# Kernel tuning notes

Measured on AMD Instinct MI355X. Metric: run time of the kernel, lower is better.

Reference implementation:

```python
import jax, jax.numpy as jnp
import numpy as np

DIM = 1024
NUM_HEADS = 16
HEAD_DIM = DIM // NUM_HEADS
SCALE = 1.0 / float(np.sqrt(HEAD_DIM))


def setup_inputs() -> dict:
    key = jax.random.key(0)
    ks = jax.random.split(key, 5)
    B, S = 2, 2048
    x = jax.random.normal(ks[0], (B, S, DIM), dtype=jnp.float32)
    qkv_w = jax.random.normal(ks[1], (3 * DIM, DIM), dtype=jnp.float32) * (1.0 / np.sqrt(DIM))
    qkv_b = jax.random.normal(ks[2], (3 * DIM,), dtype=jnp.float32) * 0.02
    proj_w = jax.random.normal(ks[3], (DIM, DIM), dtype=jnp.float32) * (1.0 / np.sqrt(DIM))
    proj_b = jax.random.normal(ks[4], (DIM,), dtype=jnp.float32) * 0.02
    return {"x": x, "qkv_w": qkv_w, "qkv_b": qkv_b, "proj_w": proj_w, "proj_b": proj_b}


def reference(x, qkv_w, qkv_b, proj_w, proj_b):
    B, S, _ = x.shape
    # qkv projection: (B,S,3*DIM) -> (3, B, H, S, Dh)
    qkv = x @ qkv_w.T + qkv_b
    qkv = qkv.reshape(B, S, 3, NUM_HEADS, HEAD_DIM).transpose(2, 0, 3, 1, 4)
    q, k, v = qkv[0], qkv[1], qkv[2]
    # scaled dot-product attention (full score matrix, as in the original)
    scores = jnp.einsum('bhqd,bhkd->bhqk', q, k) * SCALE
    attn = jax.nn.softmax(scores, axis=-1)
    out = jnp.einsum('bhqk,bhkd->bhqd', attn, v)  # (B,H,S,Dh)
    out = out.transpose(0, 2, 1, 3).reshape(B, S, DIM)
    return out @ proj_w.T + proj_b
```

## Files before the change

### kernel.cpp

```cpp
#include <hip/hip_runtime.h>

#define DIM_ 1024
#define NH_ 16
#define HD_ 64
#define B_ 2
#define S_ 2048
#define M_ (B_ * S_)
#define NQKV_ (3 * DIM_)

typedef __attribute__((ext_vector_type(8))) __bf16 bf16x8;
typedef __attribute__((ext_vector_type(4))) __bf16 bf16x4;
typedef __attribute__((ext_vector_type(4))) float f32x4;

__device__ __forceinline__ void gl_lds16(const void* g, void* l) {
  __builtin_amdgcn_global_load_lds(
      (__attribute__((address_space(1))) void*)const_cast<void*>(g),
      (__attribute__((address_space(3))) void*)l, 16, 0, 0);
}

#define N4_X 1048576
#define N4_W1 786432
#define N4_W2 262144
__global__ __launch_bounds__(256) void cast_all(const float* __restrict__ x,
                                                const float* __restrict__ w1,
                                                const float* __restrict__ w2,
                                                __bf16* __restrict__ xb,
                                                __bf16* __restrict__ w1b,
                                                __bf16* __restrict__ w2b) {
  int i = blockIdx.x * 256 + threadIdx.x;
  const int stride = gridDim.x * 256;
  for (; i < N4_X + N4_W1 + N4_W2; i += stride) {
    const float4* src;
    bf16x4* dst;
    int j;
    if (i < N4_X) { src = (const float4*)x; dst = (bf16x4*)xb; j = i; }
    else if (i < N4_X + N4_W1) { src = (const float4*)w1; dst = (bf16x4*)w1b; j = i - N4_X; }
    else { src = (const float4*)w2; dst = (bf16x4*)w2b; j = i - (N4_X + N4_W1); }
    float4 v = src[j];
    bf16x4 o;
    o[0] = (__bf16)v.x; o[1] = (__bf16)v.y; o[2] = (__bf16)v.z; o[3] = (__bf16)v.w;
    dst[j] = o;
  }
}

template <int MODE>
__global__ __launch_bounds__(256) void gemm_bt(const __bf16* __restrict__ A,
                                               const __bf16* __restrict__ Bw,
                                               const float* __restrict__ bias,
                                               __bf16* __restrict__ Qp, __bf16* __restrict__ Kp,
                                               __bf16* __restrict__ Vt, float* __restrict__ Cout) {
  constexpr int KD = 1024;
  __shared__ __bf16 As[128 * 64];
  __shared__ __bf16 Bs[128 * 64];
  const int tid = threadIdx.x;
  const int lane = tid & 63;
  const int wave = tid >> 6;
  const int quad = lane >> 4;
  const int r16 = lane & 15;
  const int wm = wave >> 1;
  const int wn = wave & 1;
  const int m0 = blockIdx.y * 128;
  const int n0 = blockIdx.x * 128;

  const f32x4 fz = {0.f, 0.f, 0.f, 0.f};
  f32x4 acc[4][4];
#pragma unroll
  for (int i = 0; i < 4; ++i)
#pragma unroll
    for (int j = 0; j < 4; ++j) acc[i][j] = fz;

  const __bf16* ga[4];
  const __bf16* gb[4];
  __bf16 *la[4], *lb[4];
#pragma unroll
  for (int i = 0; i < 4; ++i) {
    const int c = tid + i * 256;
    const int r = c >> 3, cc = c & 7;
    const int col = ((cc ^ (r & 7)) * 8);
    ga[i] = A + (size_t)(m0 + r) * KD + col;
    gb[i] = Bw + (size_t)(n0 + r) * KD + col;
    la[i] = &As[c * 8];
    lb[i] = &Bs[c * 8];
  }

  for (int kt = 0; kt < KD / 64; ++kt) {
    __syncthreads();
#pragma unroll
    for (int i = 0; i < 4; ++i) {
      gl_lds16(ga[i], la[i]); ga[i] += 64;
      gl_lds16(gb[i], lb[i]); gb[i] += 64;
    }
    __syncthreads();

    bf16x8 af[2][4], bfr[2][4];
#pragma unroll
    for (int sub = 0; sub < 2; ++sub) {
      const int ch = ((sub * 4 + quad) ^ (r16 & 7)) * 8;
#pragma unroll
      for (int mt = 0; mt < 4; ++mt)
        af[sub][mt] = *(const bf16x8*)&As[(wm * 64 + mt * 16 + r16) * 64 + ch];
#pragma unroll
      for (int nt = 0; nt < 4; ++nt)
        bfr[sub][nt] = *(const bf16x8*)&Bs[(wn * 64 + nt * 16 + r16) * 64 + ch];
    }
#pragma unroll
    for (int sub = 0; sub < 2; ++sub)
#pragma unroll
      for (int mt = 0; mt < 4; ++mt)
#pragma unroll
        for (int nt = 0; nt < 4; ++nt)
          acc[mt][nt] =
              __builtin_amdgcn_mfma_f32_16x16x32_bf16(af[sub][mt], bfr[sub][nt], acc[mt][nt], 0, 0, 0);
  }

  if (MODE == 0) {
#pragma unroll
    for (int nt = 0; nt < 4; ++nt) {
      const int n = n0 + wn * 64 + nt * 16 + r16;
      const int sel = n >> 10;
      const int h = (n >> 6) & 15;
      const int dh = n & 63;
      const float bs = bias[n];
      if (sel == 2) {
#pragma unroll
        for (int mt = 0; mt < 4; ++mt) {
          const int m = m0 + wm * 64 + mt * 16 + quad * 4;
          const int b = m >> 11;
          const int s = m & 2047;
          const int slot = (s & ~31) | (((s >> 2) & 3) << 3) | (((s >> 4) & 1) << 2);
          bf16x4 ov;
#pragma unroll
          for (int r = 0; r < 4; ++r) ov[r] = (__bf16)(acc[mt][nt][r] + bs);
          *(bf16x4*)&Vt[((size_t)((b * NH_ + h) * HD_ + dh)) * S_ + slot] = ov;
        }
      } else {
        __bf16* dst = (sel == 0) ? Qp : Kp;
        const float mul = (sel == 0) ? 0.18033688011112042f : 1.0f;
#pragma unroll
        for (int mt = 0; mt < 4; ++mt) {
#pragma unroll
          for (int r = 0; r < 4; ++r) {
            const int m = m0 + wm * 64 + mt * 16 + quad * 4 + r;
            const int b = m >> 11;
            const int s = m & 2047;
            dst[((size_t)((b * NH_ + h) * S_ + s)) * HD_ + dh] =
                (__bf16)((acc[mt][nt][r] + bs) * mul);
          }
        }
      }
    }
  } else {
#pragma unroll
    for (int nt = 0; nt < 4; ++nt) {
      const int n = n0 + wn * 64 + nt * 16 + r16;
      const float bs = bias[n];
#pragma unroll
      for (int mt = 0; mt < 4; ++mt) {
#pragma unroll
        for (int r = 0; r < 4; ++r) {
          const int m = m0 + wm * 64 + mt * 16 + quad * 4 + r;
          Cout[(size_t)m * DIM_ + n] = acc[mt][nt][r] + bs;
        }
      }
    }
  }
}

__global__ __launch_bounds__(512) void attn(const __bf16* __restrict__ Qp,
                                            const __bf16* __restrict__ Kp,
                                            const __bf16* __restrict__ Vtp,
                                            __bf16* __restrict__ ctx) {
  __shared__ __bf16 Ks[2][128 * 64];
  __shared__ __bf16 Vs[2][64 * 128];
  const int tid = threadIdx.x;
  const int lane = tid & 63;
  const int wave = tid >> 6;
  const int quad = lane >> 4;
  const int r16 = lane & 15;
  const int bh = blockIdx.y;
  const int q0 = blockIdx.x * 128;
  const int qrow = q0 + wave * 16 + r16;

  const __bf16* qb = Qp + ((size_t)bh * S_ + qrow) * HD_;
  const bf16x8 qf0 = *(const bf16x8*)(qb + quad * 8);
  const bf16x8 qf1 = *(const bf16x8*)(qb + 32 + quad * 8);

  const f32x4 fz = {0.f, 0.f, 0.f, 0.f};
  f32x4 o[4];
#pragma unroll
  for (int d = 0; d < 4; ++d) o[d] = fz;
  float lsum = 0.f;

  const __bf16* gk[2];
  const __bf16* gv[2];
  int lofs[2];
#pragma unroll
  for (int i = 0; i < 2; ++i) {
    const int c = tid + i * 512;
    const int kr = c >> 3, kc = c & 7;
    gk[i] = Kp + ((size_t)bh * S_ + kr) * HD_ + ((kc ^ (kr & 7)) * 8);
    const int vr = c >> 4, vc = c & 15;
    gv[i] = Vtp + ((size_t)bh * HD_ + vr) * S_ + ((vc ^ (vr & 15)) * 8);
    lofs[i] = c * 8;
  }

#pragma unroll
  for (int i = 0; i < 2; ++i) {
    gl_lds16(gk[i], &Ks[0][lofs[i]]); gk[i] += 128 * HD_;
    gl_lds16(gv[i], &Vs[0][lofs[i]]); gv[i] += 128;
  }

  for (int kt = 0; kt < S_ / 128; ++kt) {
    const int cb = kt & 1;
    __syncthreads();
    if (kt + 1 < S_ / 128) {
#pragma unroll
      for (int i = 0; i < 2; ++i) {
        gl_lds16(gk[i], &Ks[cb ^ 1][lofs[i]]); gk[i] += 128 * HD_;
        gl_lds16(gv[i], &Vs[cb ^ 1][lofs[i]]); gv[i] += 128;
      }
    }

    f32x4 sa[8];
#pragma unroll
    for (int mt = 0; mt < 8; ++mt) {
      const int row = mt * 16 + r16;
      bf16x8 k0 = *(const bf16x8*)&Ks[cb][row * 64 + ((quad ^ (row & 7)) * 8)];
      bf16x8 k1 = *(const bf16x8*)&Ks[cb][row * 64 + (((4 + quad) ^ (row & 7)) * 8)];
      f32x4 t = fz;
      t = __builtin_amdgcn_mfma_f32_16x16x32_bf16(k0, qf0, t, 0, 0, 0);
      t = __builtin_amdgcn_mfma_f32_16x16x32_bf16(k1, qf1, t, 0, 0, 0);
      sa[mt] = t;
    }

    bf16x8 pf[4];
#pragma unroll
    for (int ks = 0; ks < 4; ++ks)
#pragma unroll
      for (int r = 0; r < 4; ++r) {
        float p0 = __builtin_amdgcn_exp2f(sa[2 * ks][r]);
        float p1 = __builtin_amdgcn_exp2f(sa[2 * ks + 1][r]);
        lsum += p0 + p1;
        pf[ks][r] = (__bf16)p0;
        pf[ks][4 + r] = (__bf16)p1;
      }

#pragma unroll
    for (int ks = 0; ks < 4; ++ks)
#pragma unroll
      for (int dt = 0; dt < 4; ++dt) {
        const int row = dt * 16 + r16;
        bf16x8 va = *(const bf16x8*)&Vs[cb][row * 128 + (((4 * ks + quad) ^ (row & 15)) * 8)];
        o[dt] = __builtin_amdgcn_mfma_f32_16x16x32_bf16(va, pf[ks], o[dt], 0, 0, 0);
      }
  }

  lsum += __shfl_xor(lsum, 16);
  lsum += __shfl_xor(lsum, 32);
  const float inv = 1.0f / lsum;
  const int b = bh >> 4, h = bh & 15;
  const int s = q0 + wave * 16 + r16;
#pragma unroll
  for (int dt = 0; dt < 4; ++dt) {
    bf16x4 ov;
#pragma unroll
    for (int r = 0; r < 4; ++r) ov[r] = (__bf16)(o[dt][r] * inv);
    *(bf16x4*)&ctx[((size_t)(b * S_ + s)) * DIM_ + h * 64 + dt * 16 + quad * 4] = ov;
  }
}

extern "C" void kernel_launch(void* const* d_in, const int* in_sizes, int n_in, void* d_out,
                              int out_size, void* d_ws, size_t ws_size, hipStream_t stream) {
  const float* x = (const float*)d_in[0];
  const float* qkv_w = (const float*)d_in[1];
  const float* qkv_b = (const float*)d_in[2];
  const float* proj_w = (const float*)d_in[3];
  const float* proj_b = (const float*)d_in[4];
  float* out = (float*)d_out;

  char* ws = (char*)d_ws;
  __bf16* Xb = (__bf16*)(ws);
  __bf16* Wb = (__bf16*)(ws + 8388608);
  __bf16* Pb = (__bf16*)(ws + 14680064);
  __bf16* Qp = (__bf16*)(ws + 16777216);
  __bf16* Kp = (__bf16*)(ws + 25165824);
  __bf16* Vt = (__bf16*)(ws + 33554432);
  __bf16* Cx = (__bf16*)(ws + 41943040);

  cast_all<<<2048, 256, 0, stream>>>(x, qkv_w, proj_w, Xb, Wb, Pb);
  gemm_bt<0><<<dim3(NQKV_ / 128, M_ / 128), 256, 0, stream>>>(Xb, Wb, qkv_b, Qp, Kp, Vt, nullptr);
  attn<<<dim3(S_ / 128, 32), 512, 0, stream>>>(Qp, Kp, Vt, Cx);
  gemm_bt<1><<<dim3(DIM_ / 128, M_ / 128), 256, 0, stream>>>(Cx, Pb, proj_b, nullptr, nullptr,
                                                             nullptr, out);
}
```

Baseline: 186.0 us.

## Use 8-wave GEMM blocks and smaller M tiles for output projection

The bf16 GEMM kernel now runs 512 threads (8 waves) per block instead of 256, so each wave owns a smaller slice of M (MT 16-row tiles). The M tile size becomes a template parameter, and the output projection uses BM=64 to double its grid. Global-to-LDS loads are merged into one loop shared by A and B, and fragment loads are interleaved per k-substep to cut register pressure. The aim is more waves and blocks in flight to hide latency, at the cost of less register-level reuse per wave and more B-tile reloads for the smaller projection tiles.

```diff
diff --git a/kernel.cpp b/kernel.cpp
--- a/kernel.cpp
+++ b/kernel.cpp
@@ -43,15 +43,19 @@
   }
 }
 
-template <int MODE>
-__global__ __launch_bounds__(256) void gemm_bt(const __bf16* __restrict__ A,
-                                               const __bf16* __restrict__ Bw,
-                                               const float* __restrict__ bias,
-                                               __bf16* __restrict__ Qp, __bf16* __restrict__ Kp,
-                                               __bf16* __restrict__ Vt, float* __restrict__ Cout) {
+template <int MODE, int BM>
+__global__ __launch_bounds__(512, 4) void gemm_bt(const __bf16* __restrict__ A,
+                                                  const __bf16* __restrict__ Bw,
+                                                  const float* __restrict__ bias,
+                                                  __bf16* __restrict__ Qp, __bf16* __restrict__ Kp,
+                                                  __bf16* __restrict__ Vt,
+                                                  float* __restrict__ Cout) {
   constexpr int KD = 1024;
-  __shared__ __bf16 As[128 * 64];
-  __shared__ __bf16 Bs[128 * 64];
+  constexpr int BN = 128;
+  constexpr int MT = BM / 64;
+  constexpr int NC = (BM + BN) / 64;
+  __shared__ __bf16 As[BM * 64];
+  __shared__ __bf16 Bs[BN * 64];
   const int tid = threadIdx.x;
   const int lane = tid & 63;
   const int wave = tid >> 6;
@@ -59,58 +63,56 @@
   const int r16 = lane & 15;
   const int wm = wave >> 1;
   const int wn = wave & 1;
-  const int m0 = blockIdx.y * 128;
-  const int n0 = blockIdx.x * 128;
+  const int m0 = blockIdx.y * BM;
+  const int n0 = blockIdx.x * BN;
 
   const f32x4 fz = {0.f, 0.f, 0.f, 0.f};
-  f32x4 acc[4][4];
-#pragma unroll
-  for (int i = 0; i < 4; ++i)
+  f32x4 acc[MT][4];
+#pragma unroll
+  for (int i = 0; i < MT; ++i)
 #pragma unroll
     for (int j = 0; j < 4; ++j) acc[i][j] = fz;
 
-  const __bf16* ga[4];
-  const __bf16* gb[4];
-  __bf16 *la[4], *lb[4];
-#pragma unroll
-  for (int i = 0; i < 4; ++i) {
-    const int c = tid + i * 256;
-    const int r = c >> 3, cc = c & 7;
-    const int col = ((cc ^ (r & 7)) * 8);
-    ga[i] = A + (size_t)(m0 + r) * KD + col;
-    gb[i] = Bw + (size_t)(n0 + r) * KD + col;
-    la[i] = &As[c * 8];
-    lb[i] = &Bs[c * 8];
+  const __bf16* gp[NC];
+  __bf16* lp[NC];
+#pragma unroll
+  for (int i = 0; i < NC; ++i) {
+    const int c = tid + i * 512;
+    if (c < BM * 8) {
+      const int r = c >> 3, cc = c & 7;
+      gp[i] = A + (size_t)(m0 + r) * KD + ((cc ^ (r & 7)) * 8);
+      lp[i] = &As[c * 8];
+    } else {
+      const int c2 = c - BM * 8;
+      const int r = c2 >> 3, cc = c2 & 7;
+      gp[i] = Bw + (size_t)(n0 + r) * KD + ((cc ^ (r & 7)) * 8);
+      lp[i] = &Bs[c2 * 8];
+    }
   }
 
   for (int kt = 0; kt < KD / 64; ++kt) {
     __syncthreads();
 #pragma unroll
-    for (int i = 0; i < 4; ++i) {
-      gl_lds16(ga[i], la[i]); ga[i] += 64;
-      gl_lds16(gb[i], lb[i]); gb[i] += 64;
-    }
+    for (int i = 0; i < NC; ++i) { gl_lds16(gp[i], lp[i]); gp[i] += 64; }
     __syncthreads();
 
-    bf16x8 af[2][4], bfr[2][4];
 #pragma unroll
     for (int sub = 0; sub < 2; ++sub) {
       const int ch = ((sub * 4 + quad) ^ (r16 & 7)) * 8;
-#pragma unroll
-      for (int mt = 0; mt < 4; ++mt)
-        af[sub][mt] = *(const bf16x8*)&As[(wm * 64 + mt * 16 + r16) * 64 + ch];
+      bf16x8 af[MT], bfr[4];
+#pragma unroll
+      for (int mt = 0; mt < MT; ++mt)
+        af[mt] = *(const bf16x8*)&As[(wm * MT * 16 + mt * 16 + r16) * 64 + ch];
 #pragma unroll
       for (int nt = 0; nt < 4; ++nt)
-        bfr[sub][nt] = *(const bf16x8*)&Bs[(wn * 64 + nt * 16 + r16) * 64 + ch];
-    }
-#pragma unroll
-    for (int sub = 0; sub < 2; ++sub)
-#pragma unroll
-      for (int mt = 0; mt < 4; ++mt)
+        bfr[nt] = *(const bf16x8*)&Bs[(wn * 64 + nt * 16 + r16) * 64 + ch];
+#pragma unroll
+      for (int mt = 0; mt < MT; ++mt)
 #pragma unroll
         for (int nt = 0; nt < 4; ++nt)
           acc[mt][nt] =
-              __builtin_amdgcn_mfma_f32_16x16x32_bf16(af[sub][mt], bfr[sub][nt], acc[mt][nt], 0, 0, 0);
+              __builtin_amdgcn_mfma_f32_16x16x32_bf16(af[mt], bfr[nt], acc[mt][nt], 0, 0, 0);
+    }
   }
 
   if (MODE == 0) {
@@ -123,8 +125,8 @@
       const float bs = bias[n];
       if (sel == 2) {
 #pragma unroll
-        for (int mt = 0; mt < 4; ++mt) {
-          const int m = m0 + wm * 64 + mt * 16 + quad * 4;
+        for (int mt = 0; mt < MT; ++mt) {
+          const int m = m0 + wm * MT * 16 + mt * 16 + quad * 4;
           const int b = m >> 11;
           const int s = m & 2047;
           const int slot = (s & ~31) | (((s >> 2) & 3) << 3) | (((s >> 4) & 1) << 2);
@@ -137,10 +139,10 @@
         __bf16* dst = (sel == 0) ? Qp : Kp;
         const float mul = (sel == 0) ? 0.18033688011112042f : 1.0f;
 #pragma unroll
-        for (int mt = 0; mt < 4; ++mt) {
+        for (int mt = 0; mt < MT; ++mt) {
 #pragma unroll
           for (int r = 0; r < 4; ++r) {
-            const int m = m0 + wm * 64 + mt * 16 + quad * 4 + r;
+            const int m = m0 + wm * MT * 16 + mt * 16 + quad * 4 + r;
             const int b = m >> 11;
             const int s = m & 2047;
             dst[((size_t)((b * NH_ + h) * S_ + s)) * HD_ + dh] =
@@ -155,10 +157,10 @@
       const int n = n0 + wn * 64 + nt * 16 + r16;
       const float bs = bias[n];
 #pragma unroll
-      for (int mt = 0; mt < 4; ++mt) {
+      for (int mt = 0; mt < MT; ++mt) {
 #pragma unroll
         for (int r = 0; r < 4; ++r) {
-          const int m = m0 + wm * 64 + mt * 16 + quad * 4 + r;
+          const int m = m0 + wm * MT * 16 + mt * 16 + quad * 4 + r;
           Cout[(size_t)m * DIM_ + n] = acc[mt][nt][r] + bs;
         }
       }
@@ -288,8 +290,9 @@
   __bf16* Cx = (__bf16*)(ws + 41943040);
 
   cast_all<<<2048, 256, 0, stream>>>(x, qkv_w, proj_w, Xb, Wb, Pb);
-  gemm_bt<0><<<dim3(NQKV_ / 128, M_ / 128), 256, 0, stream>>>(Xb, Wb, qkv_b, Qp, Kp, Vt, nullptr);
+  gemm_bt<0, 128><<<dim3(NQKV_ / 128, M_ / 128), 512, 0, stream>>>(Xb, Wb, qkv_b, Qp, Kp, Vt,
+                                                                   nullptr);
   attn<<<dim3(S_ / 128, 32), 512, 0, stream>>>(Qp, Kp, Vt, Cx);
-  gemm_bt<1><<<dim3(DIM_ / 128, M_ / 128), 256, 0, stream>>>(Cx, Pb, proj_b, nullptr, nullptr,
-                                                             nullptr, out);
-}
+  gemm_bt<1, 64><<<dim3(DIM_ / 128, M_ / 64), 512, 0, stream>>>(Cx, Pb, proj_b, nullptr, nullptr,
+                                                                nullptr, out);
+}
```

Measured after the change: 171.4 us. 1.09x faster.
